# Kernel tuning notes

Hardware: AMD Instinct MI355X
Metric: run time of the kernel (lower is better)

## Reference

```python
import jax, jax.numpy as jnp
import numpy as np

EMBED_DIM = 192
N_HEADS = 8
HEAD_DIM = EMBED_DIM // N_HEADS  # 24


def setup_inputs() -> dict:
    key = jax.random.key(0)
    k1, k2, k3 = jax.random.split(key, 3)
    b, n = 32, 1024
    s_in = 1.0 / np.sqrt(EMBED_DIM)
    return {
        "x": jax.random.normal(k1, (b, n, EMBED_DIM), dtype=jnp.float32),
        "W_qkv": jax.random.normal(k2, (EMBED_DIM, 3 * EMBED_DIM), dtype=jnp.float32) * s_in,
        "b_qkv": jnp.zeros((3 * EMBED_DIM,), dtype=jnp.float32),
        "W_proj": jax.random.normal(k3, (EMBED_DIM, EMBED_DIM), dtype=jnp.float32) * s_in,
        "b_proj": jnp.zeros((EMBED_DIM,), dtype=jnp.float32),
    }


def reference(x, W_qkv, b_qkv, W_proj, b_proj):
    b, n, _ = x.shape
    qkv = x @ W_qkv + b_qkv                               # [b, n, 3*E]
    qkv = qkv.reshape(b, n, 3, N_HEADS, HEAD_DIM)
    qkv = jnp.transpose(qkv, (2, 0, 3, 1, 4))             # [3, b, h, n, d]
    q, k, v = qkv[0], qkv[1], qkv[2]
    scale = 1.0 / np.sqrt(HEAD_DIM)
    scores = jnp.einsum("bhqd,bhkd->bhqk", q, k) * scale  # [b, h, n, n]
    attn = jax.nn.softmax(scores, axis=-1)
    # dropout is identity in eval mode
    out = jnp.einsum("bhqk,bhkd->bhqd", attn, v)          # [b, h, n, d]
    out = jnp.transpose(out, (0, 2, 1, 3)).reshape(b, n, EMBED_DIM)
    return out @ W_proj + b_proj
```

## Files before the change

### kernel.cpp

```cpp
#include <hip/hip_runtime.h>
#include <hip/hip_bf16.h>
#include <math.h>

#define B_ 32
#define N_ 1024
#define E_ 192
#define H_ 8
#define D_ 24
#define DP_ 32
#define M_ (B_ * N_)
#define QK_ELEMS ((size_t)B_ * H_ * N_ * DP_)
#define SC2 0.29448889f

typedef short bf16x8 __attribute__((ext_vector_type(8)));
typedef float f32x4 __attribute__((ext_vector_type(4)));
typedef unsigned int u32;
typedef unsigned short u16;

__device__ __forceinline__ u16 bf16_rne(float x) {
    u32 u = __builtin_bit_cast(u32, x);
    u += 0x7FFFu + ((u >> 16) & 1u);
    return (u16)(u >> 16);
}
__device__ __forceinline__ u32 cvt_pk(float lo, float hi) {
    u32 r;
    asm("v_cvt_pk_bf16_f32 %0, %1, %2" : "=v"(r) : "v"(lo), "v"(hi));
    return r;
}
__device__ __forceinline__ float fast_exp2(float x) {
#if __has_builtin(__builtin_amdgcn_exp2f)
    return __builtin_amdgcn_exp2f(x);
#else
    return __expf(x * 0.6931471805599453f);
#endif
}
__device__ __forceinline__ void gload16(const void* g, void* l) {
    __builtin_amdgcn_global_load_lds(
        (const __attribute__((address_space(1))) void*)g,
        (__attribute__((address_space(3))) void*)l, 16, 0, 0);
}

__global__ __launch_bounds__(256) void convert_k(const float* __restrict__ x,
                                                 const float* __restrict__ wqkv,
                                                 const float* __restrict__ wproj,
                                                 u16* __restrict__ xb,
                                                 u16* __restrict__ wqkvt,
                                                 u16* __restrict__ wprojt,
                                                 u16* __restrict__ vb) {
    const int b = blockIdx.x;
    const int t = threadIdx.x;
    if (b < 3072) {
        const size_t base = ((size_t)b * 256 + t) * 8;
        const float4 a = *(const float4*)(x + base);
        const float4 c = *(const float4*)(x + base + 4);
        const uint4 o = make_uint4(cvt_pk(a.x, a.y), cvt_pk(a.z, a.w),
                                   cvt_pk(c.x, c.y), cvt_pk(c.z, c.w));
        *(uint4*)(xb + base) = o;
    } else if (b < 3072 + 432) {
        const int idx = (b - 3072) * 256 + t;
        const int n = idx / 192, k = idx - n * 192;
        wqkvt[idx] = bf16_rne(wqkv[(size_t)k * 576 + n]);
    } else if (b < 3072 + 432 + 144) {
        const int idx = (b - 3504) * 256 + t;
        const int n = idx / 192, k = idx - n * 192;
        wprojt[idx] = bf16_rne(wproj[(size_t)k * 192 + n]);
    } else {
        const int p = b - 3648;
        const int bh = p >> 2;
        const int d = 24 + ((p & 3) << 1) + ((t * 8) >> 10);
        const int n = (t * 8) & 1023;
        const u32 v = (d == 31) ? 0x3F803F80u : 0u;
        const uint4 o = make_uint4(v, v, v, v);
        *(uint4*)(vb + ((size_t)bh << 15) + ((size_t)d << 10) + n) = o;
    }
}

template <int MODE>
__global__ __launch_bounds__(256) void gemm2(const u16* __restrict__ Ab,
                                             const u16* __restrict__ Bt,
                                             const float* __restrict__ bias,
                                             u16* __restrict__ qb,
                                             u16* __restrict__ kb,
                                             u16* __restrict__ vb,
                                             float* __restrict__ outp) {
    __shared__ u16 smem[128 * 64 + 64 * 64];
    u16* As = smem;
    u16* Bs = smem + 128 * 64;

    const int tid = threadIdx.x;
    const int w = tid >> 6, lane = tid & 63, g = lane >> 4, q15 = lane & 15;
    const int wm = w >> 1, wn = w & 1;
    const int m0 = blockIdx.y * 128, n0 = blockIdx.x * 64;

    f32x4 acc[4][2];
    #pragma unroll
    for (int i = 0; i < 4; ++i)
        #pragma unroll
        for (int j = 0; j < 2; ++j) acc[i][j] = (f32x4){0.f, 0.f, 0.f, 0.f};

    for (int k0 = 0; k0 < 192; k0 += 64) {
        #pragma unroll
        for (int is = 0; is < 4; ++is) {
            const int lb = w * 256 + is * 64;
            const int li = lb + lane;
            const int row = li >> 3;
            const int sl = (li & 7) ^ (row & 7);
            gload16(Ab + (size_t)(m0 + row) * 192 + k0 + sl * 8, As + lb * 8);
        }
        #pragma unroll
        for (int is = 0; is < 2; ++is) {
            const int lb = w * 128 + is * 64;
            const int li = lb + lane;
            const int row = li >> 3;
            const int sl = (li & 7) ^ (row & 7);
            gload16(Bt + (size_t)(n0 + row) * 192 + k0 + sl * 8, Bs + lb * 8);
        }
        __syncthreads();
        #pragma unroll
        for (int kk = 0; kk < 2; ++kk) {
            const int sw = (kk * 4 + g) ^ (q15 & 7);
            const bf16x8 b0 = *(const bf16x8*)(Bs + (wn * 32 + q15) * 64 + sw * 8);
            const bf16x8 b1 = *(const bf16x8*)(Bs + (wn * 32 + 16 + q15) * 64 + sw * 8);
            #pragma unroll
            for (int mi = 0; mi < 4; ++mi) {
                const bf16x8 a = *(const bf16x8*)(As + (wm * 64 + mi * 16 + q15) * 64 + sw * 8);
                acc[mi][0] = __builtin_amdgcn_mfma_f32_16x16x32_bf16(a, b0, acc[mi][0], 0, 0, 0);
                acc[mi][1] = __builtin_amdgcn_mfma_f32_16x16x32_bf16(a, b1, acc[mi][1], 0, 0, 0);
            }
        }
        __syncthreads();
    }

    if (MODE == 1) {
        #pragma unroll
        for (int mi = 0; mi < 4; ++mi) {
            const int m = m0 + wm * 64 + mi * 16 + g * 4;
            #pragma unroll
            for (int ni = 0; ni < 2; ++ni) {
                const int n = n0 + wn * 32 + ni * 16 + q15;
                const float bv = bias[n];
                #pragma unroll
                for (int r = 0; r < 4; ++r)
                    outp[(size_t)(m + r) * 192 + n] = acc[mi][ni][r] + bv;
            }
        }
        return;
    }

    const int tensor = n0 / 192;
    const int rem0 = n0 - tensor * 192;
    if (tensor < 2) {
        u16* dst = (tensor == 0) ? qb : kb;
        #pragma unroll
        for (int mi = 0; mi < 4; ++mi) {
            const int m = m0 + wm * 64 + mi * 16 + g * 4;
            #pragma unroll
            for (int ni = 0; ni < 2; ++ni) {
                const int cl = wn * 32 + ni * 16 + q15;
                const int rem = rem0 + cl;
                const int h = rem / 24, d = rem - h * 24;
                const float bv = bias[n0 + cl];
                #pragma unroll
                for (int r = 0; r < 4; ++r) {
                    const int mm = m + r;
                    const int bb = mm >> 10, nn = mm & 1023;
                    float val = acc[mi][ni][r] + bv;
                    if (tensor == 0) val *= SC2;
                    const size_t base = ((size_t)(bb * H_ + h) << 15) + ((size_t)nn << 5);
                    dst[base + d] = bf16_rne(val);
                    if (d >= 16) dst[base + d + 8] = 0;
                }
            }
        }
    } else {
        u16* Vb = smem;
        #pragma unroll
        for (int mi = 0; mi < 4; ++mi) {
            const int ml = wm * 64 + mi * 16 + g * 4;
            #pragma unroll
            for (int ni = 0; ni < 2; ++ni) {
                const int cl = wn * 32 + ni * 16 + q15;
                const float bv = bias[n0 + cl];
                #pragma unroll
                for (int r = 0; r < 4; ++r)
                    Vb[cl * 136 + ml + r] = bf16_rne(acc[mi][ni][r] + bv);
            }
        }
        __syncthreads();
        const int lc = tid >> 2, seg = tid & 3;
        const int rem = rem0 + lc;
        const int h = rem / 24, d = rem - h * 24;
        const int bb = m0 >> 10, nnb = m0 & 1023;
        const u16* src = Vb + lc * 136 + seg * 32;
        u16* gdst = vb + (((size_t)(bb * H_ + h)) << 15) + ((size_t)d << 10) + nnb + seg * 32;
        #pragma unroll
        for (int q = 0; q < 4; ++q)
            *(uint4*)(gdst + q * 8) = *(const uint4*)(src + q * 8);
    }
}

__global__ __launch_bounds__(256) void attn_mfma(const u16* __restrict__ qb,
                                                 const u16* __restrict__ kb,
                                                 const u16* __restrict__ vb,
                                                 u16* __restrict__ ctxb) {
    __shared__ u16 Kl[64 * 40];
    __shared__ u16 Vt[32 * 72];
    __shared__ u16 Pl[4 * 16 * 72];

    const int bh = blockIdx.x;
    const int qt = blockIdx.y;
    const int tid = threadIdx.x;
    const int w = tid >> 6;
    const int lane = tid & 63;
    const int g = lane >> 4;
    const int q15 = lane & 15;

    const u16* qg = qb + (((size_t)bh * N_ + qt * 64 + w * 16) << 5);
    const u16* kg = kb + ((size_t)bh << 15);
    const u16* vg = vb + ((size_t)bh << 15);

    const bf16x8 qf = *(const bf16x8*)(qg + (q15 << 5) + g * 8);

    f32x4 acc0 = {0.f, 0.f, 0.f, 0.f};
    f32x4 acc1 = {0.f, 0.f, 0.f, 0.f};
    float m_run = -INFINITY, l_run = 0.f;
    u16* Pw = Pl + w * 16 * 72;

    const int krow = tid >> 2, kslot = tid & 3;
    const int vrow = tid >> 3, vslot = tid & 7;

    for (int j0 = 0; j0 < N_; j0 += 64) {
        __syncthreads();
        *(bf16x8*)(Kl + krow * 40 + kslot * 8) =
            *(const bf16x8*)(kg + ((j0 + krow) << 5) + kslot * 8);
        *(bf16x8*)(Vt + vrow * 72 + vslot * 8) =
            *(const bf16x8*)(vg + (vrow << 10) + j0 + vslot * 8);
        __syncthreads();

        f32x4 s0, s1, s2, s3;
        {
            const bf16x8 kf0 = *(const bf16x8*)(Kl + (0 + q15) * 40 + g * 8);
            const bf16x8 kf1 = *(const bf16x8*)(Kl + (16 + q15) * 40 + g * 8);
            const bf16x8 kf2 = *(const bf16x8*)(Kl + (32 + q15) * 40 + g * 8);
            const bf16x8 kf3 = *(const bf16x8*)(Kl + (48 + q15) * 40 + g * 8);
            const f32x4 z = {0.f, 0.f, 0.f, 0.f};
            s0 = __builtin_amdgcn_mfma_f32_16x16x32_bf16(kf0, qf, z, 0, 0, 0);
            s1 = __builtin_amdgcn_mfma_f32_16x16x32_bf16(kf1, qf, z, 0, 0, 0);
            s2 = __builtin_amdgcn_mfma_f32_16x16x32_bf16(kf2, qf, z, 0, 0, 0);
            s3 = __builtin_amdgcn_mfma_f32_16x16x32_bf16(kf3, qf, z, 0, 0, 0);
        }
        float p[16];
        #pragma unroll
        for (int r = 0; r < 4; ++r) {
            p[0 + r]  = s0[r];
            p[4 + r]  = s1[r];
            p[8 + r]  = s2[r];
            p[12 + r] = s3[r];
        }

        const float ma = fmaxf(fmaxf(p[0], p[1]), fmaxf(p[2], p[3]));
        const float mb = fmaxf(fmaxf(p[4], p[5]), fmaxf(p[6], p[7]));
        const float mc = fmaxf(fmaxf(p[8], p[9]), fmaxf(p[10], p[11]));
        const float md = fmaxf(fmaxf(p[12], p[13]), fmaxf(p[14], p[15]));
        float mloc = fmaxf(fmaxf(ma, mb), fmaxf(mc, md));
        mloc = fmaxf(mloc, __shfl_xor(mloc, 16));
        mloc = fmaxf(mloc, __shfl_xor(mloc, 32));

        if (!__all(mloc - m_run <= 8.f)) {
            const float m_new = fmaxf(m_run, mloc);
            const float corr = fast_exp2(m_run - m_new);
            m_run = m_new;
            l_run *= corr;
            #pragma unroll
            for (int r = 0; r < 4; ++r) {
                const float c = __shfl(corr, (g << 2) | r);
                acc0[r] *= c;
                acc1[r] *= c;
            }
        }

        float psum = 0.f;
        #pragma unroll
        for (int i = 0; i < 16; ++i) {
            p[i] = fast_exp2(p[i] - m_run);
            psum += p[i];
        }
        psum += __shfl_xor(psum, 16);
        psum += __shfl_xor(psum, 32);
        l_run += psum;

        #pragma unroll
        for (int t4 = 0; t4 < 4; ++t4) {
            uint2 wv;
            wv.x = cvt_pk(p[t4 * 4 + 0], p[t4 * 4 + 1]);
            wv.y = cvt_pk(p[t4 * 4 + 2], p[t4 * 4 + 3]);
            *(uint2*)(Pw + q15 * 72 + t4 * 16 + g * 4) = wv;
        }

        #pragma unroll
        for (int hf = 0; hf < 2; ++hf) {
            const bf16x8 pa = *(const bf16x8*)(Pw + q15 * 72 + hf * 32 + g * 8);
            const bf16x8 v0 = *(const bf16x8*)(Vt + q15 * 72 + hf * 32 + g * 8);
            const bf16x8 v1 = *(const bf16x8*)(Vt + (16 + q15) * 72 + hf * 32 + g * 8);
            acc0 = __builtin_amdgcn_mfma_f32_16x16x32_bf16(pa, v0, acc0, 0, 0, 0);
            acc1 = __builtin_amdgcn_mfma_f32_16x16x32_bf16(pa, v1, acc1, 0, 0, 0);
        }
    }

    const float inv = 1.f / l_run;
    const int bb = bh >> 3, hh = bh & 7;
    #pragma unroll
    for (int r = 0; r < 4; ++r) {
        const float iv = __shfl(inv, (g << 2) | r);
        const int row = qt * 64 + w * 16 + g * 4 + r;
        u16* dst = ctxb + ((size_t)bb * N_ + row) * E_ + hh * D_;
        dst[q15] = bf16_rne(acc0[r] * iv);
        if (q15 < 8) dst[16 + q15] = bf16_rne(acc1[r] * iv);
    }
}

extern "C" void kernel_launch(void* const* d_in, const int* in_sizes, int n_in,
                              void* d_out, int out_size, void* d_ws, size_t ws_size,
                              hipStream_t stream) {
    const float* x     = (const float*)d_in[0];
    const float* Wqkv  = (const float*)d_in[1];
    const float* bqkv  = (const float*)d_in[2];
    const float* Wproj = (const float*)d_in[3];
    const float* bproj = (const float*)d_in[4];
    float* out = (float*)d_out;

    u16* xb     = (u16*)d_ws;
    u16* wqkvt  = xb + (size_t)M_ * E_;
    u16* wprojt = wqkvt + 576 * 192;
    u16* qb     = wprojt + 192 * 192;
    u16* kb     = qb + QK_ELEMS;
    u16* vb     = kb + QK_ELEMS;
    u16* ctxb   = vb + QK_ELEMS;

    dim3 blk(256);
    convert_k<<<4672, blk, 0, stream>>>(x, Wqkv, Wproj, xb, wqkvt, wprojt, vb);
    gemm2<0><<<dim3(9, 256), blk, 0, stream>>>(xb, wqkvt, bqkv, qb, kb, vb, nullptr);
    attn_mfma<<<dim3(B_ * H_, N_ / 64), blk, 0, stream>>>(qb, kb, vb, ctxb);
    gemm2<1><<<dim3(3, 256), blk, 0, stream>>>(ctxb, wprojt, bproj,
                                               nullptr, nullptr, nullptr, out);
}
```

Measured before the change: 206.0 us.

## Fold max subtraction into MFMA accumulator and compute row sum via V column

The running max is now seeded by passing -m_run as the MFMA accumulator input, so scores come out already shifted and the per-element subtraction disappears. The running denominator is no longer summed with shuffles. It is read at the end from a padded V column (column 15 of the second tile), which presumably holds ones, so the PV MFMA accumulates the row sum for free. The rescale path now triggers only when a score exceeds the threshold and starts m_run at 0, which risks overflow behaviour if scores are large or the ones column is not set up.

```diff
diff --git a/kernel.cpp b/kernel.cpp
--- a/kernel.cpp
+++ b/kernel.cpp
@@ -223,7 +223,7 @@
 
     f32x4 acc0 = {0.f, 0.f, 0.f, 0.f};
     f32x4 acc1 = {0.f, 0.f, 0.f, 0.f};
-    float m_run = -INFINITY, l_run = 0.f;
+    float m_run = 0.f;
     u16* Pw = Pl + w * 16 * 72;
 
     const int krow = tid >> 2, kslot = tid & 3;
@@ -239,62 +239,59 @@
 
         f32x4 s0, s1, s2, s3;
         {
+            const f32x4 cin = {-m_run, -m_run, -m_run, -m_run};
             const bf16x8 kf0 = *(const bf16x8*)(Kl + (0 + q15) * 40 + g * 8);
             const bf16x8 kf1 = *(const bf16x8*)(Kl + (16 + q15) * 40 + g * 8);
             const bf16x8 kf2 = *(const bf16x8*)(Kl + (32 + q15) * 40 + g * 8);
             const bf16x8 kf3 = *(const bf16x8*)(Kl + (48 + q15) * 40 + g * 8);
-            const f32x4 z = {0.f, 0.f, 0.f, 0.f};
-            s0 = __builtin_amdgcn_mfma_f32_16x16x32_bf16(kf0, qf, z, 0, 0, 0);
-            s1 = __builtin_amdgcn_mfma_f32_16x16x32_bf16(kf1, qf, z, 0, 0, 0);
-            s2 = __builtin_amdgcn_mfma_f32_16x16x32_bf16(kf2, qf, z, 0, 0, 0);
-            s3 = __builtin_amdgcn_mfma_f32_16x16x32_bf16(kf3, qf, z, 0, 0, 0);
-        }
-        float p[16];
-        #pragma unroll
-        for (int r = 0; r < 4; ++r) {
-            p[0 + r]  = s0[r];
-            p[4 + r]  = s1[r];
-            p[8 + r]  = s2[r];
-            p[12 + r] = s3[r];
-        }
-
-        const float ma = fmaxf(fmaxf(p[0], p[1]), fmaxf(p[2], p[3]));
-        const float mb = fmaxf(fmaxf(p[4], p[5]), fmaxf(p[6], p[7]));
-        const float mc = fmaxf(fmaxf(p[8], p[9]), fmaxf(p[10], p[11]));
-        const float md = fmaxf(fmaxf(p[12], p[13]), fmaxf(p[14], p[15]));
-        float mloc = fmaxf(fmaxf(ma, mb), fmaxf(mc, md));
+            s0 = __builtin_amdgcn_mfma_f32_16x16x32_bf16(kf0, qf, cin, 0, 0, 0);
+            s1 = __builtin_amdgcn_mfma_f32_16x16x32_bf16(kf1, qf, cin, 0, 0, 0);
+            s2 = __builtin_amdgcn_mfma_f32_16x16x32_bf16(kf2, qf, cin, 0, 0, 0);
+            s3 = __builtin_amdgcn_mfma_f32_16x16x32_bf16(kf3, qf, cin, 0, 0, 0);
+        }
+
+        const float a0 = fmaxf(fmaxf(s0[0], s0[1]), fmaxf(s0[2], s0[3]));
+        const float a1 = fmaxf(fmaxf(s1[0], s1[1]), fmaxf(s1[2], s1[3]));
+        const float a2 = fmaxf(fmaxf(s2[0], s2[1]), fmaxf(s2[2], s2[3]));
+        const float a3 = fmaxf(fmaxf(s3[0], s3[1]), fmaxf(s3[2], s3[3]));
+        float mloc = fmaxf(fmaxf(a0, a1), fmaxf(a2, a3));
         mloc = fmaxf(mloc, __shfl_xor(mloc, 16));
         mloc = fmaxf(mloc, __shfl_xor(mloc, 32));
 
-        if (!__all(mloc - m_run <= 8.f)) {
-            const float m_new = fmaxf(m_run, mloc);
-            const float corr = fast_exp2(m_run - m_new);
-            m_run = m_new;
-            l_run *= corr;
+        if (__builtin_expect(__any(mloc > 8.f), 0)) {
+            const float delta = fmaxf(mloc, 0.f);
+            m_run += delta;
+            const float corr = fast_exp2(-delta);
             #pragma unroll
             for (int r = 0; r < 4; ++r) {
                 const float c = __shfl(corr, (g << 2) | r);
                 acc0[r] *= c;
                 acc1[r] *= c;
             }
-        }
-
-        float psum = 0.f;
-        #pragma unroll
-        for (int i = 0; i < 16; ++i) {
-            p[i] = fast_exp2(p[i] - m_run);
-            psum += p[i];
-        }
-        psum += __shfl_xor(psum, 16);
-        psum += __shfl_xor(psum, 32);
-        l_run += psum;
-
-        #pragma unroll
-        for (int t4 = 0; t4 < 4; ++t4) {
-            uint2 wv;
-            wv.x = cvt_pk(p[t4 * 4 + 0], p[t4 * 4 + 1]);
-            wv.y = cvt_pk(p[t4 * 4 + 2], p[t4 * 4 + 3]);
-            *(uint2*)(Pw + q15 * 72 + t4 * 16 + g * 4) = wv;
+            #pragma unroll
+            for (int r = 0; r < 4; ++r) {
+                s0[r] -= delta; s1[r] -= delta; s2[r] -= delta; s3[r] -= delta;
+            }
+        }
+
+        #pragma unroll
+        for (int r = 0; r < 4; ++r) {
+            s0[r] = fast_exp2(s0[r]);
+            s1[r] = fast_exp2(s1[r]);
+            s2[r] = fast_exp2(s2[r]);
+            s3[r] = fast_exp2(s3[r]);
+        }
+
+        {
+            uint2 w0, w1, w2, w3;
+            w0.x = cvt_pk(s0[0], s0[1]); w0.y = cvt_pk(s0[2], s0[3]);
+            w1.x = cvt_pk(s1[0], s1[1]); w1.y = cvt_pk(s1[2], s1[3]);
+            w2.x = cvt_pk(s2[0], s2[1]); w2.y = cvt_pk(s2[2], s2[3]);
+            w3.x = cvt_pk(s3[0], s3[1]); w3.y = cvt_pk(s3[2], s3[3]);
+            *(uint2*)(Pw + q15 * 72 + 0  + g * 4) = w0;
+            *(uint2*)(Pw + q15 * 72 + 16 + g * 4) = w1;
+            *(uint2*)(Pw + q15 * 72 + 32 + g * 4) = w2;
+            *(uint2*)(Pw + q15 * 72 + 48 + g * 4) = w3;
         }
 
         #pragma unroll
@@ -307,11 +304,11 @@
         }
     }
 
-    const float inv = 1.f / l_run;
     const int bb = bh >> 3, hh = bh & 7;
     #pragma unroll
     for (int r = 0; r < 4; ++r) {
-        const float iv = __shfl(inv, (g << 2) | r);
+        const float l = __shfl(acc1[r], (g << 4) | 15);
+        const float iv = 1.f / l;
         const int row = qt * 64 + w * 16 + g * 4 + r;
         u16* dst = ctxb + ((size_t)bb * N_ + row) * E_ + hh * D_;
         dst[q15] = bf16_rne(acc0[r] * iv);
```

New measurement: 198.8 us. -3.5%, faster.
